# Kernel tuning notes

Hardware: AMD Instinct MI355X
Metric: run time of the kernel (lower is better)

## Reference

```python
import jax, jax.numpy as jnp
import numpy as np

N = 100_000      # nodes
E = 1_600_000    # edges (avg degree 16)
F_IN = 165       # Elliptic node features
HID = 64         # hidden_units
NCLS = 2         # num_classes
NEG_SLOPE = 0.2  # PyG GATConv default


def setup_inputs() -> dict:
    key = jax.random.key(0)
    ks = jax.random.split(key, 9)
    x = jax.random.normal(ks[0], (N, F_IN), jnp.float32)
    edge_index = jax.random.randint(ks[1], (2, E), 0, N, jnp.int32)
    W1 = jax.random.normal(ks[2], (F_IN, HID), jnp.float32) / np.sqrt(F_IN)
    a1_src = jax.random.normal(ks[3], (HID,), jnp.float32) / np.sqrt(HID)
    a1_dst = jax.random.normal(ks[4], (HID,), jnp.float32) / np.sqrt(HID)
    b1 = jnp.zeros((HID,), jnp.float32)
    W2 = jax.random.normal(ks[5], (HID, NCLS), jnp.float32) / np.sqrt(HID)
    a2_src = jax.random.normal(ks[6], (NCLS,), jnp.float32) / np.sqrt(NCLS)
    a2_dst = jax.random.normal(ks[7], (NCLS,), jnp.float32) / np.sqrt(NCLS)
    b2 = jnp.zeros((NCLS,), jnp.float32)
    return {"x": x, "edge_index": edge_index, "W1": W1, "a1_src": a1_src,
            "a1_dst": a1_dst, "b1": b1, "W2": W2, "a2_src": a2_src,
            "a2_dst": a2_dst, "b2": b2}


def gat_layer(x, src, dst, W, a_s, a_d, b, n):
    # h: [N, out]; per-edge attention e_ij = LeakyReLU(a_s.h_j + a_d.h_i)
    h = x @ W
    e = jax.nn.leaky_relu((h @ a_s)[src] + (h @ a_d)[dst], NEG_SLOPE)
    # numerically stable segment softmax over incoming edges of each dst node
    emax = jax.ops.segment_max(e, dst, num_segments=n)
    ee = jnp.exp(e - jax.lax.stop_gradient(emax)[dst])
    denom = jax.ops.segment_sum(ee, dst, num_segments=n)
    alpha = ee / denom[dst]                       # [E_tot]
    out = jax.ops.segment_sum(alpha[:, None] * h[src], dst, num_segments=n)
    return out + b


def reference(x, edge_index, W1, a1_src, a1_dst, b1, W2, a2_src, a2_dst, b2):
    n = x.shape[0]
    loops = jnp.arange(n, dtype=edge_index.dtype)   # PyG add_self_loops=True
    src = jnp.concatenate([edge_index[0], loops])
    dst = jnp.concatenate([edge_index[1], loops])
    h = jax.nn.relu(gat_layer(x, src, dst, W1, a1_src, a1_dst, b1, n))
    # F.dropout(training=False) is identity in eval mode
    out = gat_layer(h, src, dst, W2, a2_src, a2_dst, b2, n)
    return out, edge_index
```

## Files before the change

kernel.cpp:

```cpp
#include <hip/hip_runtime.h>
#include <hip/hip_bf16.h>
#include <math.h>

#define N_NODES 100000
#define N_EDGES 1600000
#define F_IN 165
#define HID 64
#define SLOPE 0.2f

#define NBUCK 196
#define BSHIFT 9
#define BMASK 511
#define NBLK 256
#define CHUNK 6250
#define MSCAN (NBUCK * NBLK)

typedef short short8 __attribute__((ext_vector_type(8)));
typedef float f32x4 __attribute__((ext_vector_type(4)));
typedef float f32x2 __attribute__((ext_vector_type(2)));

__device__ __forceinline__ float lrelu(float x) { return x > 0.f ? x : SLOPE * x; }

__device__ __forceinline__ unsigned short f2bf(float f) {
    unsigned u = __float_as_uint(f);
    u += 0x7FFFu + ((u >> 16) & 1u);
    return (unsigned short)(u >> 16);
}
__device__ __forceinline__ float bflo(unsigned u) { return __uint_as_float(u << 16); }
__device__ __forceinline__ float bfhi(unsigned u) { return __uint_as_float(u & 0xFFFF0000u); }
__device__ __forceinline__ unsigned char f2fp8(float f) {
    return (unsigned char)(__builtin_amdgcn_cvt_pk_fp8_f32(f, f, 0, false) & 0xFF);
}

__global__ __launch_bounds__(256) void k_hist(const int* __restrict__ ei,
                                              int* __restrict__ hist,
                                              float* __restrict__ out_edges,
                                              const float* __restrict__ W1,
                                              unsigned short* __restrict__ Wsw) {
    int blk = blockIdx.x, t = threadIdx.x;
    int idx = blk * 256 + t;
    if (idx < 12288) {
        int j = idx & 7;
        int r = idx >> 3;
        int n = r & 15; r >>= 4;
        int tt = r & 3; r >>= 2;
        int q = r & 3;  int c = r >> 2;
        int k = c * 32 + q * 8 + j;
        int col = tt * 16 + n;
        float v = (k < F_IN) ? W1[k * HID + col] : 0.f;
        Wsw[idx] = f2bf(v);
    }
    __shared__ int h[NBUCK];
    for (int j = t; j < NBUCK; j += 256) h[j] = 0;
    __syncthreads();
    int i0 = blk * CHUNK, i1 = i0 + CHUNK;
    for (int i = i0 + t * 2; i < i1; i += 512) {
        int2 sv = *(const int2*)&ei[i];
        int2 dv = *(const int2*)&ei[N_EDGES + i];
        *(float2*)&out_edges[i] = make_float2((float)sv.x, (float)sv.y);
        *(float2*)&out_edges[N_EDGES + i] = make_float2((float)dv.x, (float)dv.y);
        atomicAdd(&h[dv.x >> BSHIFT], 1);
        atomicAdd(&h[dv.y >> BSHIFT], 1);
    }
    __syncthreads();
    for (int j = t; j < NBUCK; j += 256) hist[j * NBLK + blk] = h[j];
}

#define ASTRIDE 200
__global__ __launch_bounds__(256, 4) void k_gemm1(const float* __restrict__ x,
                                                  const unsigned short* __restrict__ Wsw,
                                                  const float* __restrict__ a1s,
                                                  const float* __restrict__ a1d,
                                                  unsigned char* __restrict__ h1,
                                                  float* __restrict__ s1,
                                                  float* __restrict__ d1) {
    __shared__ unsigned short Ah[64 * ASTRIDE];
    const int tid = threadIdx.x;
    const int base = blockIdx.x * 64;

    for (int i = tid; i < 64 * 35; i += 256) {
        int nl = i / 35, kk = 165 + (i - nl * 35);
        Ah[nl * ASTRIDE + kk] = 0;
    }
    const int fbase = base * F_IN;
    const int flim = N_NODES * F_IN;
    for (int i = tid; i < (64 * F_IN) / 4; i += 256) {
        int f = fbase + i * 4;
        float vv[4];
        if (f + 4 <= flim) {
            float4 v = *(const float4*)&x[f];
            vv[0] = v.x; vv[1] = v.y; vv[2] = v.z; vv[3] = v.w;
        } else {
#pragma unroll
            for (int e = 0; e < 4; e++) vv[e] = (f + e < flim) ? x[f + e] : 0.f;
        }
#pragma unroll
        for (int e = 0; e < 4; e++) {
            int g = f + e;
            int node = g / F_IN;
            int kk = g - node * F_IN;
            Ah[(node - base) * ASTRIDE + kk] = f2bf(vv[e]);
        }
    }
    __syncthreads();

    const int lane = tid & 63;
    const int w = tid >> 6;
    const int m16 = lane & 15;
    const int q = lane >> 4;
    f32x4 acc[4];
#pragma unroll
    for (int t = 0; t < 4; t++) acc[t] = (f32x4){0.f, 0.f, 0.f, 0.f};

    const unsigned short* arow = &Ah[(w * 16 + m16) * ASTRIDE];
    const short8* Wsw8 = (const short8*)Wsw;
#pragma unroll
    for (int c = 0; c < 6; c++) {
        short8 a = *(const short8*)&arow[c * 32 + q * 8];
#pragma unroll
        for (int t = 0; t < 4; t++) {
            short8 b = Wsw8[(c * 4 + q) * 64 + t * 16 + m16];
            acc[t] = __builtin_amdgcn_mfma_f32_16x16x32_bf16(a, b, acc[t], 0, 0, 0);
        }
    }

    float as_l[4], ad_l[4];
#pragma unroll
    for (int t = 0; t < 4; t++) { as_l[t] = a1s[t * 16 + m16]; ad_l[t] = a1d[t * 16 + m16]; }
#pragma unroll
    for (int r = 0; r < 4; r++) {
        int node = base + w * 16 + q * 4 + r;
        bool ok = node < N_NODES;
        float ps = 0.f, pd = 0.f;
#pragma unroll
        for (int t = 0; t < 4; t++) {
            float v = acc[t][r];
            if (ok) h1[(size_t)node * HID + t * 16 + m16] = f2fp8(v);
            ps += v * as_l[t];
            pd += v * ad_l[t];
        }
#pragma unroll
        for (int off = 1; off < 16; off <<= 1) {
            ps += __shfl_xor(ps, off);
            pd += __shfl_xor(pd, off);
        }
        if (ok && m16 == 0) { s1[node] = ps; d1[node] = pd; }
    }
}

__global__ void k_scan1(int* __restrict__ a, int* __restrict__ bsum) {
    __shared__ int sd[256];
    int i = blockIdx.x * 256 + threadIdx.x;
    int v = a[i];
    sd[threadIdx.x] = v;
    __syncthreads();
    for (int off = 1; off < 256; off <<= 1) {
        int t = (threadIdx.x >= off) ? sd[threadIdx.x - off] : 0;
        __syncthreads();
        sd[threadIdx.x] += t;
        __syncthreads();
    }
    a[i] = sd[threadIdx.x] - v;
    if (threadIdx.x == 255) bsum[blockIdx.x] = sd[255];
}

__global__ void k_scan2(int* __restrict__ bsum, int nb) {
    __shared__ int sd[256];
    int t = threadIdx.x;
    int v = (t < nb) ? bsum[t] : 0;
    sd[t] = v;
    __syncthreads();
    for (int off = 1; off < 256; off <<= 1) {
        int u = (t >= off) ? sd[t - off] : 0;
        __syncthreads();
        sd[t] += u;
        __syncthreads();
    }
    if (t < nb) bsum[t] = sd[t] - v;
}

__global__ __launch_bounds__(256) void k_part(const int* __restrict__ ei,
                                              const int* __restrict__ off,
                                              const int* __restrict__ bsum,
                                              unsigned* __restrict__ pairs) {
    __shared__ int base_s[NBUCK];
    __shared__ int cnt[NBUCK];
    int blk = blockIdx.x, t = threadIdx.x;
    for (int j = t; j < NBUCK; j += 256) {
        base_s[j] = off[j * NBLK + blk] + bsum[j];
        cnt[j] = 0;
    }
    __syncthreads();
    int i0 = blk * CHUNK, i1 = i0 + CHUNK;
    for (int i = i0 + t * 2; i < i1; i += 512) {
        int2 sv = *(const int2*)&ei[i];
        int2 dv = *(const int2*)&ei[N_EDGES + i];
        int b0 = dv.x >> BSHIFT;
        int p0 = base_s[b0] + atomicAdd(&cnt[b0], 1);
        pairs[p0] = ((unsigned)sv.x << BSHIFT) | (unsigned)(dv.x & BMASK);
        int b1v = dv.y >> BSHIFT;
        int p1 = base_s[b1v] + atomicAdd(&cnt[b1v], 1);
        pairs[p1] = ((unsigned)sv.y << BSHIFT) | (unsigned)(dv.y & BMASK);
    }
}

__global__ __launch_bounds__(512) void k_build2(const unsigned* __restrict__ pairs,
                                                const int* __restrict__ off,
                                                const int* __restrict__ bsum,
                                                int* __restrict__ row_ptr,
                                                int* __restrict__ deg,
                                                int* __restrict__ csr) {
    __shared__ int hcnt[512];
    __shared__ int cur[512];
    int b = blockIdx.x, t = threadIdx.x;
    hcnt[t] = 0;
    __syncthreads();
    int rs = off[b * NBLK] + bsum[b];
    int re = (b == NBUCK - 1) ? N_EDGES : off[(b + 1) * NBLK] + bsum[b + 1];
    for (int j = rs + t; j < re; j += 512)
        atomicAdd(&hcnt[pairs[j] & BMASK], 1);
    __syncthreads();
    int v = hcnt[t];
    cur[t] = v;
    __syncthreads();
    for (int o = 1; o < 512; o <<= 1) {
        int u = (t >= o) ? cur[t - o] : 0;
        __syncthreads();
        cur[t] += u;
        __syncthreads();
    }
    int excl = cur[t] - v;
    __syncthreads();
    cur[t] = rs + excl;
    int node = b * 512 + t;
    if (node < N_NODES) {
        row_ptr[node] = rs + excl;
        deg[node] = v;
    }
    __syncthreads();
    for (int j = rs + t; j < re; j += 512) {
        unsigned p = pairs[j];
        int pos = atomicAdd(&cur[p & BMASK], 1);
        csr[pos] = (int)(p >> BSHIFT);
    }
}

__global__ __launch_bounds__(256, 8) void k_agg1(const unsigned char* __restrict__ h1,
                                                 const float* __restrict__ s1,
                                                 const float* __restrict__ d1,
                                                 const int* __restrict__ row_ptr,
                                                 const int* __restrict__ deg,
                                                 const int* __restrict__ csr,
                                                 const float* __restrict__ b1,
                                                 const float* __restrict__ W2,
                                                 const float* __restrict__ a2s,
                                                 const float* __restrict__ a2d,
                                                 uint2* __restrict__ node2,
                                                 float* __restrict__ d2arr) {
    int wid = (blockIdx.x * blockDim.x + threadIdx.x) >> 6;
    int lane = threadIdx.x & 63;
    if (wid >= N_NODES) return;
    int slot = lane >> 4;
    int cg = lane & 15;
    float di = d1[wid];
    float dpart = 0.f;
    float4 acc = make_float4(0.f, 0.f, 0.f, 0.f);
    int rs = row_ptr[wid], re = rs + deg[wid];
    for (int b = rs; b < re; b += 64) {
        int j = b + lane;
        int srcl = 0;
        float eel = 0.f;
        if (j < re) {
            srcl = csr[j];
            eel = __expf(lrelu(s1[srcl] + di));
        }
        int cnt = re - b; if (cnt > 64) cnt = 64;
        int tmax = (cnt + 3) >> 2;
        for (int t = 0; t < tmax; t += 4) {
            int n = tmax - t; if (n > 4) n = 4;
            int s0 = 0, s1i = 0, s2i = 0, s3i = 0;
            float e0 = 0.f, e1 = 0.f, e2 = 0.f, e3 = 0.f;
            s0 = __shfl(srcl, (t + 0) * 4 + slot);
            e0 = __shfl(eel, (t + 0) * 4 + slot);
            if (n > 1) { s1i = __shfl(srcl, (t + 1) * 4 + slot); e1 = __shfl(eel, (t + 1) * 4 + slot); }
            if (n > 2) { s2i = __shfl(srcl, (t + 2) * 4 + slot); e2 = __shfl(eel, (t + 2) * 4 + slot); }
            if (n > 3) { s3i = __shfl(srcl, (t + 3) * 4 + slot); e3 = __shfl(eel, (t + 3) * 4 + slot); }
            unsigned u0 = 0, u1 = 0, u2 = 0, u3 = 0;
            u0 = *(const unsigned*)&h1[((size_t)s0 << 6) + cg * 4];
            if (n > 1) u1 = *(const unsigned*)&h1[((size_t)s1i << 6) + cg * 4];
            if (n > 2) u2 = *(const unsigned*)&h1[((size_t)s2i << 6) + cg * 4];
            if (n > 3) u3 = *(const unsigned*)&h1[((size_t)s3i << 6) + cg * 4];
            {
                f32x2 lo = __builtin_amdgcn_cvt_pk_f32_fp8((int)u0, false);
                f32x2 hi = __builtin_amdgcn_cvt_pk_f32_fp8((int)u0, true);
                dpart += e0;
                acc.x += e0 * lo.x; acc.y += e0 * lo.y;
                acc.z += e0 * hi.x; acc.w += e0 * hi.y;
            }
            if (n > 1) {
                f32x2 lo = __builtin_amdgcn_cvt_pk_f32_fp8((int)u1, false);
                f32x2 hi = __builtin_amdgcn_cvt_pk_f32_fp8((int)u1, true);
                dpart += e1;
                acc.x += e1 * lo.x; acc.y += e1 * lo.y;
                acc.z += e1 * hi.x; acc.w += e1 * hi.y;
            }
            if (n > 2) {
                f32x2 lo = __builtin_amdgcn_cvt_pk_f32_fp8((int)u2, false);
                f32x2 hi = __builtin_amdgcn_cvt_pk_f32_fp8((int)u2, true);
                dpart += e2;
                acc.x += e2 * lo.x; acc.y += e2 * lo.y;
                acc.z += e2 * hi.x; acc.w += e2 * hi.y;
            }
            if (n > 3) {
                f32x2 lo = __builtin_amdgcn_cvt_pk_f32_fp8((int)u3, false);
                f32x2 hi = __builtin_amdgcn_cvt_pk_f32_fp8((int)u3, true);
                dpart += e3;
                acc.x += e3 * lo.x; acc.y += e3 * lo.y;
                acc.z += e3 * hi.x; acc.w += e3 * hi.y;
            }
        }
    }
#pragma unroll
    for (int off = 16; off < 64; off <<= 1) {
        acc.x += __shfl_xor(acc.x, off);
        acc.y += __shfl_xor(acc.y, off);
        acc.z += __shfl_xor(acc.z, off);
        acc.w += __shfl_xor(acc.w, off);
        dpart += __shfl_xor(dpart, off);
    }
    float ees = __expf(lrelu(s1[wid] + di));
    unsigned us = *(const unsigned*)&h1[((size_t)wid << 6) + cg * 4];
    f32x2 slo = __builtin_amdgcn_cvt_pk_f32_fp8((int)us, false);
    f32x2 shi = __builtin_amdgcn_cvt_pk_f32_fp8((int)us, true);
    float denom = dpart + ees;
    acc.x += ees * slo.x; acc.y += ees * slo.y;
    acc.z += ees * shi.x; acc.w += ees * shi.y;
    float inv = 1.f / denom;
    float4 bb = *(const float4*)&b1[cg * 4];
    float o0 = fmaxf(acc.x * inv + bb.x, 0.f);
    float o1 = fmaxf(acc.y * inv + bb.y, 0.f);
    float o2 = fmaxf(acc.z * inv + bb.z, 0.f);
    float o3 = fmaxf(acc.w * inv + bb.w, 0.f);
    float2 w0 = *(const float2*)&W2[(cg * 4 + 0) * 2];
    float2 w1 = *(const float2*)&W2[(cg * 4 + 1) * 2];
    float2 w2 = *(const float2*)&W2[(cg * 4 + 2) * 2];
    float2 w3 = *(const float2*)&W2[(cg * 4 + 3) * 2];
    float p0 = o0 * w0.x + o1 * w1.x + o2 * w2.x + o3 * w3.x;
    float p1 = o0 * w0.y + o1 * w1.y + o2 * w2.y + o3 * w3.y;
#pragma unroll
    for (int off = 1; off < 16; off <<= 1) {
        p0 += __shfl_xor(p0, off);
        p1 += __shfl_xor(p1, off);
    }
    if (lane == 0) {
        float s2 = p0 * a2s[0] + p1 * a2s[1];
        float d2v = p0 * a2d[0] + p1 * a2d[1];
        unsigned pk = (unsigned)f2bf(p0) | ((unsigned)f2bf(p1) << 16);
        node2[wid] = make_uint2(pk, __float_as_uint(s2));
        d2arr[wid] = d2v;
    }
}

__global__ __launch_bounds__(256) void k_agg2(const uint2* __restrict__ node2,
                                              const float* __restrict__ d2arr,
                                              const int* __restrict__ row_ptr,
                                              const int* __restrict__ deg,
                                              const int* __restrict__ csr,
                                              const float* __restrict__ b2,
                                              float* __restrict__ out) {
    int wid = (blockIdx.x * blockDim.x + threadIdx.x) >> 6;
    int lane = threadIdx.x & 63;
    int node = wid * 4 + (lane >> 4);
    int eg = lane & 15;
    if (node >= N_NODES) return;
    uint2 vi = node2[node];
    float d2 = d2arr[node];
    float denom = 0.f, p0 = 0.f, p1 = 0.f;
    int rs = row_ptr[node], re = rs + deg[node];
    for (int j = rs + eg; j < re; j += 16) {
        int s = csr[j];
        uint2 v = node2[s];
        float ee = __expf(lrelu(__uint_as_float(v.y) + d2));
        denom += ee;
        p0 += ee * bflo(v.x);
        p1 += ee * bfhi(v.x);
    }
#pragma unroll
    for (int off = 1; off < 16; off <<= 1) {
        denom += __shfl_xor(denom, off);
        p0 += __shfl_xor(p0, off);
        p1 += __shfl_xor(p1, off);
    }
    if (eg == 0) {
        float ee = __expf(lrelu(__uint_as_float(vi.y) + d2));
        denom += ee;
        p0 += ee * bflo(vi.x);
        p1 += ee * bfhi(vi.x);
        out[(size_t)node * 2 + 0] = p0 / denom + b2[0];
        out[(size_t)node * 2 + 1] = p1 / denom + b2[1];
    }
}

extern "C" void kernel_launch(void* const* d_in, const int* in_sizes, int n_in,
                              void* d_out, int out_size, void* d_ws, size_t ws_size,
                              hipStream_t stream) {
    const float* x   = (const float*)d_in[0];
    const int*   ei  = (const int*)d_in[1];
    const float* W1  = (const float*)d_in[2];
    const float* a1s = (const float*)d_in[3];
    const float* a1d = (const float*)d_in[4];
    const float* b1  = (const float*)d_in[5];
    const float* W2  = (const float*)d_in[6];
    const float* a2s = (const float*)d_in[7];
    const float* a2d = (const float*)d_in[8];
    const float* b2  = (const float*)d_in[9];
    float* out = (float*)d_out;

    unsigned char* h1 = (unsigned char*)d_ws;
    float* s1      = (float*)(h1 + (size_t)N_NODES * HID);
    float* d1      = s1 + N_NODES;
    float* d2arr   = d1 + N_NODES;
    uint2* node2   = (uint2*)(d2arr + N_NODES);
    int* row_ptr   = (int*)(node2 + N_NODES);
    int* deg       = row_ptr + N_NODES;
    int* off       = deg + N_NODES;
    int* bsum      = off + MSCAN + 64;
    int* csr       = bsum + 256;
    unsigned* pairs = (unsigned*)(csr + N_EDGES);
    unsigned short* Wsw = (unsigned short*)(pairs + N_EDGES);

    k_hist<<<NBLK, 256, 0, stream>>>(ei, off, out + 2 * N_NODES, W1, Wsw);
    k_gemm1<<<(N_NODES + 63) / 64, 256, 0, stream>>>(x, Wsw, a1s, a1d, h1, s1, d1);
    k_scan1<<<MSCAN / 256, 256, 0, stream>>>(off, bsum);
    k_scan2<<<1, 256, 0, stream>>>(bsum, MSCAN / 256);
    k_part<<<NBLK, 256, 0, stream>>>(ei, off, bsum, pairs);
    k_build2<<<NBUCK, 512, 0, stream>>>(pairs, off, bsum, row_ptr, deg, csr);
    k_agg1<<<N_NODES / 4, 256, 0, stream>>>(h1, s1, d1, row_ptr, deg, csr,
                                            b1, W2, a2s, a2d, node2, d2arr);
    k_agg2<<<(N_NODES + 15) / 16, 256, 0, stream>>>(node2, d2arr, row_ptr, deg, csr, b2, out);
}
```

Measured before the change: 229.2 us.

## Map four nodes per wavefront in layer-1 aggregation with 8-edge batched gathers

Layer-1 aggregation now gives each 16-lane group its own destination node instead of one node per 64-lane wavefront. Each group loops over its node's edges in batches of 8, with every lane redundantly loading the csr index and computing the attention exponent, then issuing 8 independent fp8 row gathers. This removes the cross-lane shuffles and the final cross-slot reduction, and quadruples nodes per wave, aimed at low-degree nodes (about 17 edges on average). The tradeoff is redundant index and exp work across the 16 lanes, plus divergence between groups whose nodes have different degrees.

```diff
diff --git a/kernel.cpp b/kernel.cpp
--- a/kernel.cpp
+++ b/kernel.cpp
@@ -257,79 +257,43 @@
                                                  const float* __restrict__ a2d,
                                                  uint2* __restrict__ node2,
                                                  float* __restrict__ d2arr) {
-    int wid = (blockIdx.x * blockDim.x + threadIdx.x) >> 6;
+    int gwid = (blockIdx.x * blockDim.x + threadIdx.x) >> 6;
     int lane = threadIdx.x & 63;
-    if (wid >= N_NODES) return;
-    int slot = lane >> 4;
+    int node = gwid * 4 + (lane >> 4);
     int cg = lane & 15;
-    float di = d1[wid];
+    if (node >= N_NODES) return;
+    float di = d1[node];
+    int rs = row_ptr[node], re = rs + deg[node];
     float dpart = 0.f;
     float4 acc = make_float4(0.f, 0.f, 0.f, 0.f);
-    int rs = row_ptr[wid], re = rs + deg[wid];
-    for (int b = rs; b < re; b += 64) {
-        int j = b + lane;
-        int srcl = 0;
-        float eel = 0.f;
-        if (j < re) {
-            srcl = csr[j];
-            eel = __expf(lrelu(s1[srcl] + di));
-        }
-        int cnt = re - b; if (cnt > 64) cnt = 64;
-        int tmax = (cnt + 3) >> 2;
-        for (int t = 0; t < tmax; t += 4) {
-            int n = tmax - t; if (n > 4) n = 4;
-            int s0 = 0, s1i = 0, s2i = 0, s3i = 0;
-            float e0 = 0.f, e1 = 0.f, e2 = 0.f, e3 = 0.f;
-            s0 = __shfl(srcl, (t + 0) * 4 + slot);
-            e0 = __shfl(eel, (t + 0) * 4 + slot);
-            if (n > 1) { s1i = __shfl(srcl, (t + 1) * 4 + slot); e1 = __shfl(eel, (t + 1) * 4 + slot); }
-            if (n > 2) { s2i = __shfl(srcl, (t + 2) * 4 + slot); e2 = __shfl(eel, (t + 2) * 4 + slot); }
-            if (n > 3) { s3i = __shfl(srcl, (t + 3) * 4 + slot); e3 = __shfl(eel, (t + 3) * 4 + slot); }
-            unsigned u0 = 0, u1 = 0, u2 = 0, u3 = 0;
-            u0 = *(const unsigned*)&h1[((size_t)s0 << 6) + cg * 4];
-            if (n > 1) u1 = *(const unsigned*)&h1[((size_t)s1i << 6) + cg * 4];
-            if (n > 2) u2 = *(const unsigned*)&h1[((size_t)s2i << 6) + cg * 4];
-            if (n > 3) u3 = *(const unsigned*)&h1[((size_t)s3i << 6) + cg * 4];
-            {
-                f32x2 lo = __builtin_amdgcn_cvt_pk_f32_fp8((int)u0, false);
-                f32x2 hi = __builtin_amdgcn_cvt_pk_f32_fp8((int)u0, true);
-                dpart += e0;
-                acc.x += e0 * lo.x; acc.y += e0 * lo.y;
-                acc.z += e0 * hi.x; acc.w += e0 * hi.y;
-            }
-            if (n > 1) {
-                f32x2 lo = __builtin_amdgcn_cvt_pk_f32_fp8((int)u1, false);
-                f32x2 hi = __builtin_amdgcn_cvt_pk_f32_fp8((int)u1, true);
-                dpart += e1;
-                acc.x += e1 * lo.x; acc.y += e1 * lo.y;
-                acc.z += e1 * hi.x; acc.w += e1 * hi.y;
-            }
-            if (n > 2) {
-                f32x2 lo = __builtin_amdgcn_cvt_pk_f32_fp8((int)u2, false);
-                f32x2 hi = __builtin_amdgcn_cvt_pk_f32_fp8((int)u2, true);
-                dpart += e2;
-                acc.x += e2 * lo.x; acc.y += e2 * lo.y;
-                acc.z += e2 * hi.x; acc.w += e2 * hi.y;
-            }
-            if (n > 3) {
-                f32x2 lo = __builtin_amdgcn_cvt_pk_f32_fp8((int)u3, false);
-                f32x2 hi = __builtin_amdgcn_cvt_pk_f32_fp8((int)u3, true);
-                dpart += e3;
-                acc.x += e3 * lo.x; acc.y += e3 * lo.y;
-                acc.z += e3 * hi.x; acc.w += e3 * hi.y;
-            }
-        }
-    }
-#pragma unroll
-    for (int off = 16; off < 64; off <<= 1) {
-        acc.x += __shfl_xor(acc.x, off);
-        acc.y += __shfl_xor(acc.y, off);
-        acc.z += __shfl_xor(acc.z, off);
-        acc.w += __shfl_xor(acc.w, off);
-        dpart += __shfl_xor(dpart, off);
-    }
-    float ees = __expf(lrelu(s1[wid] + di));
-    unsigned us = *(const unsigned*)&h1[((size_t)wid << 6) + cg * 4];
+    const unsigned char* hb = h1 + cg * 4;
+
+    for (int j0 = rs; j0 < re; j0 += 8) {
+        int sv[8]; float ev[8];
+#pragma unroll
+        for (int k = 0; k < 8; k++) {
+            int jk = j0 + k;
+            int jc = jk < re ? jk : (re - 1);
+            sv[k] = csr[jc];
+            float e = __expf(lrelu(s1[sv[k]] + di));
+            ev[k] = (jk < re) ? e : 0.f;
+        }
+        unsigned uv[8];
+#pragma unroll
+        for (int k = 0; k < 8; k++)
+            uv[k] = *(const unsigned*)&hb[(size_t)sv[k] << 6];
+#pragma unroll
+        for (int k = 0; k < 8; k++) {
+            f32x2 lo = __builtin_amdgcn_cvt_pk_f32_fp8((int)uv[k], false);
+            f32x2 hi = __builtin_amdgcn_cvt_pk_f32_fp8((int)uv[k], true);
+            dpart += ev[k];
+            acc.x += ev[k] * lo.x; acc.y += ev[k] * lo.y;
+            acc.z += ev[k] * hi.x; acc.w += ev[k] * hi.y;
+        }
+    }
+
+    float ees = __expf(lrelu(s1[node] + di));
+    unsigned us = *(const unsigned*)&hb[(size_t)node << 6];
     f32x2 slo = __builtin_amdgcn_cvt_pk_f32_fp8((int)us, false);
     f32x2 shi = __builtin_amdgcn_cvt_pk_f32_fp8((int)us, true);
     float denom = dpart + ees;
@@ -352,12 +316,12 @@
         p0 += __shfl_xor(p0, off);
         p1 += __shfl_xor(p1, off);
     }
-    if (lane == 0) {
+    if (cg == 0) {
         float s2 = p0 * a2s[0] + p1 * a2s[1];
         float d2v = p0 * a2d[0] + p1 * a2d[1];
         unsigned pk = (unsigned)f2bf(p0) | ((unsigned)f2bf(p1) << 16);
-        node2[wid] = make_uint2(pk, __float_as_uint(s2));
-        d2arr[wid] = d2v;
+        node2[node] = make_uint2(pk, __float_as_uint(s2));
+        d2arr[node] = d2v;
     }
 }
 
@@ -435,7 +399,7 @@
     k_scan2<<<1, 256, 0, stream>>>(bsum, MSCAN / 256);
     k_part<<<NBLK, 256, 0, stream>>>(ei, off, bsum, pairs);
     k_build2<<<NBUCK, 512, 0, stream>>>(pairs, off, bsum, row_ptr, deg, csr);
-    k_agg1<<<N_NODES / 4, 256, 0, stream>>>(h1, s1, d1, row_ptr, deg, csr,
-                                            b1, W2, a2s, a2d, node2, d2arr);
+    k_agg1<<<(N_NODES + 15) / 16, 256, 0, stream>>>(h1, s1, d1, row_ptr, deg, csr,
+                                                    b1, W2, a2s, a2d, node2, d2arr);
     k_agg2<<<(N_NODES + 15) / 16, 256, 0, stream>>>(node2, d2arr, row_ptr, deg, csr, b2, out);
 }
```

Measured after the change: 210.8 us. 1.09x faster.
